# Kernel tuning notes

Measured on AMD Instinct MI355X. Metric: run time of the kernel, lower is better.

## Reference

```python
import jax, jax.numpy as jnp
import numpy as np

B, TOPK, MN = 128, 32, 64
MAX_NODES, H, E = 256, 128, 128
N_ENT, N_REL = 40000, 400


def setup_inputs() -> dict:
    key = jax.random.key(0)
    ks = jax.random.split(key, 11)
    s = 0.02  # weight init scale
    return {
        "node_embeddings": jax.random.normal(ks[0], (B, MAX_NODES + 2, H), jnp.float32),
        "entity_table": jax.random.normal(ks[1], (N_ENT, E), jnp.float32) * s,
        "relation_table": jax.random.normal(ks[2], (N_REL, E), jnp.float32) * s,
        "W_ih": jax.random.normal(ks[3], (3 * H, 2 * E), jnp.float32) * s,
        "W_hh": jax.random.normal(ks[4], (3 * H, H), jnp.float32) * s,
        "b_ih": jax.random.normal(ks[5], (3 * H,), jnp.float32) * s,
        "b_hh": jax.random.normal(ks[6], (3 * H,), jnp.float32) * s,
        "aim_nodes": jax.random.randint(ks[7], (B, TOPK), 0, MAX_NODES),
        "aim_entities": jax.random.randint(ks[8], (B, TOPK), 0, N_ENT),
        "neighbors": jax.random.randint(ks[9], (B, TOPK, MN, 2), 0, MAX_NODES + 2),
        "neighbors_num": jax.random.randint(ks[10], (B, TOPK), 0, MN + 1),
    }


def reference(node_embeddings, entity_table, relation_table, W_ih, W_hh, b_ih, b_hh,
              aim_nodes, aim_entities, neighbors, neighbors_num):
    # Agent.aggregate with use_rnn=True; returns updated node_embeddings.
    b, topk, mn, _ = neighbors.shape
    h_dim = node_embeddings.shape[-1]
    nb_nodes = neighbors[..., 0]      # (B, topk, mn) node positions
    nb_rel = neighbors[..., 1]        # (B, topk, mn) relation ids

    # per-batch gather of hidden states of neighbor nodes -> (B, topk, mn, H)
    h = jnp.take_along_axis(node_embeddings,
                            nb_nodes.reshape(b, topk * mn)[:, :, None],
                            axis=1).reshape(b, topk, mn, h_dim)
    ent = entity_table[aim_entities]          # (B, topk, E)
    rel = relation_table[nb_rel]              # (B, topk, mn, E)
    # GRU input: concat(aim entity embedding broadcast over neighbors, relation emb)
    x = jnp.concatenate(
        [jnp.broadcast_to(ent[:, :, None, :], rel.shape), rel], axis=-1)  # (B,topk,mn,2E)

    # torch GRUCell: gates ordered (r, z, n)
    gi = jnp.einsum('btme,ge->btmg', x, W_ih) + b_ih  # (B,topk,mn,3H)
    gh = jnp.einsum('btmh,gh->btmg', h, W_hh) + b_hh
    i_r, i_z, i_n = jnp.split(gi, 3, axis=-1)
    h_r, h_z, h_n = jnp.split(gh, 3, axis=-1)
    r = jax.nn.sigmoid(i_r + h_r)
    z = jax.nn.sigmoid(i_z + h_z)
    n = jnp.tanh(i_n + r * h_n)
    h_new = (1.0 - z) * n + z * h              # (B,topk,mn,H)

    # masked mean over valid neighbors (masked_fill(0) then sum / max(num,1))
    mask = jnp.arange(mn)[None, None, :] < neighbors_num[:, :, None]
    denom = neighbors_num.astype(h_new.dtype) + (neighbors_num == 0).astype(h_new.dtype)
    upd = jnp.where(mask[..., None], h_new, 0.0).sum(axis=2) / denom[..., None]  # (B,topk,H)

    # scatter updated representations back into the node table
    bidx = jnp.arange(b)[:, None]
    return node_embeddings.at[bidx, aim_nodes].set(upd)
```

## Files before the change

kernel.cpp:

```cpp
#include <hip/hip_runtime.h>

#define BB     128
#define TOPK   32
#define MN     64
#define NODES  258
#define HD     128
#define G3     384
#define NREL   400
#define SEG1_OFF 448
#define SEG2_OFF 4544
#define NROWS_TOT 37568

typedef __bf16 bf16x8 __attribute__((ext_vector_type(8)));
typedef float  f32x4  __attribute__((ext_vector_type(4)));

__device__ inline unsigned short f2bf(float f) {
    unsigned u = __float_as_uint(f);
    u = (u + 0x7fff + ((u >> 16) & 1)) >> 16;
    return (unsigned short)u;
}
__device__ inline float bf2f(unsigned short s) {
    return __uint_as_float(((unsigned)s) << 16);
}
__device__ inline float fsig(float x) {
    float e = __builtin_amdgcn_exp2f(-1.442695041f * x);
    return __builtin_amdgcn_rcpf(1.f + e);
}
__device__ inline float ftanh(float x) {
    x = fminf(15.f, fmaxf(-15.f, x));
    float e = __builtin_amdgcn_exp2f(2.885390082f * x);
    return (e - 1.f) * __builtin_amdgcn_rcpf(e + 1.f);
}

__global__ __launch_bounds__(256) void pack_all(
        const float* __restrict__ node_emb, const float* __restrict__ ent_tab,
        const float* __restrict__ rel_tab, const int* __restrict__ aim_ent,
        unsigned short* __restrict__ A, float* __restrict__ out) {
    int i = blockIdx.x * 256 + threadIdx.x;
    int row = i >> 7, k = i & 127;
    float v;
    if (row < NREL)            v = rel_tab[i];
    else if (row < SEG1_OFF)   v = 0.f;
    else if (row < SEG2_OFF)   v = ent_tab[(size_t)aim_ent[row - SEG1_OFF] * 128 + k];
    else {
        int n = row - SEG2_OFF;
        v = node_emb[(size_t)n * 128 + k];
        out[(size_t)n * 128 + k] = v;
    }
    A[i] = f2bf(v);
}

__global__ __launch_bounds__(256) void pack_w(
        const float* __restrict__ W_ih, const float* __restrict__ W_hh,
        const float* __restrict__ b_ih, const float* __restrict__ b_hh,
        unsigned short* __restrict__ Wpack, float* __restrict__ biasb) {
    int i = blockIdx.x * 256 + threadIdx.x;
    int s = i / 49152, r = i % 49152;
    int n = r >> 7, k = r & 127;
    float v;
    if (s == 0)      v = W_ih[n * 256 + 128 + k];
    else if (s == 1) v = W_ih[n * 256 + k];
    else             v = W_hh[n * 128 + k];
    Wpack[i] = f2bf(v);
    if (i < 3 * 384) {
        int s2 = i / 384, g = i % 384;
        biasb[i] = (s2 == 0) ? 0.f : (s2 == 1 ? b_ih[g] : b_hh[g]);
    }
}

__global__ __launch_bounds__(256) void mfma_gemm(
        const unsigned short* __restrict__ A, const unsigned short* __restrict__ Wpack,
        const float* __restrict__ biasb, unsigned short* __restrict__ G) {
    const int w = threadIdx.x >> 6, lane = threadIdx.x & 63;
    const int row0 = blockIdx.x * 64 + w * 16;
    const int seg  = (row0 < SEG1_OFF) ? 0 : (row0 < SEG2_OFF ? 1 : 2);
    const unsigned short* Wt = Wpack + (size_t)seg * 384 * 128;
    const int limit = (seg == 0) ? NREL : NROWS_TOT;

    const int koff  = (lane >> 4) << 3;
    const int arow  = row0 + (lane & 15);
    const int rbase = row0 + ((lane >> 4) << 2);
    bf16x8 a[4];
#pragma unroll
    for (int kb = 0; kb < 4; ++kb)
        a[kb] = *reinterpret_cast<const bf16x8*>(A + (size_t)arow * 128 + kb * 32 + koff);

#pragma unroll 2
    for (int t = 0; t < 24; ++t) {
        const int bcol = t * 16 + (lane & 15);
        bf16x8 bf[4];
#pragma unroll
        for (int kb = 0; kb < 4; ++kb)
            bf[kb] = *reinterpret_cast<const bf16x8*>(Wt + (size_t)bcol * 128 + kb * 32 + koff);
        f32x4 acc = {0.f, 0.f, 0.f, 0.f};
#pragma unroll
        for (int kb = 0; kb < 4; ++kb)
            acc = __builtin_amdgcn_mfma_f32_16x16x32_bf16(a[kb], bf[kb], acc, 0, 0, 0);
        const float bv = biasb[seg * 384 + bcol];
#pragma unroll
        for (int i = 0; i < 4; ++i) {
            int grow = rbase + i;
            if (grow < limit) G[(size_t)grow * 384 + bcol] = f2bf(acc[i] + bv);
        }
    }
}

__global__ __launch_bounds__(128) void gru_agg(
        const float* __restrict__ node_emb, const unsigned short* __restrict__ G,
        const int* __restrict__ aim_nodes, const int* __restrict__ neighbors,
        const int* __restrict__ nb_num, float* __restrict__ out) {
    const int bt = blockIdx.x;
    const int b = bt >> 5, t = bt & 31;
    const int h = threadIdx.x;

    const int myaim = aim_nodes[bt];
    for (int t2 = t + 1; t2 < TOPK; ++t2)
        if (aim_nodes[b * TOPK + t2] == myaim) return;

    __shared__ int2 nbs[MN];
    if (h < MN) nbs[h] = ((const int2*)(neighbors + (size_t)bt * MN * 2))[h];
    __syncthreads();

    const size_t erow = (size_t)(SEG1_OFF + bt) * 384;
    const float ge_r = bf2f(G[erow + h]);
    const float ge_z = bf2f(G[erow + 128 + h]);
    const float ge_n = bf2f(G[erow + 256 + h]);

    int num = nb_num[bt];
    num = (num < 0) ? 0 : (num > MN ? MN : num);

    const unsigned short* ghb = G + (size_t)(SEG2_OFF + b * NODES) * 384;
    const float* heb = node_emb + (size_t)b * NODES * 128;

    float acc = 0.f;
    int m = 0;
    for (; m + 4 <= num; m += 4) {
        float gr_r[4], gr_z[4], gr_n[4], h_r[4], h_z[4], h_n[4], hv[4];
#pragma unroll
        for (int j = 0; j < 4; ++j) {
            int2 p = nbs[m + j];
            const unsigned short* gr = G + (size_t)p.y * 384;
            const unsigned short* gh = ghb + (size_t)p.x * 384;
            gr_r[j] = bf2f(gr[h]); gr_z[j] = bf2f(gr[128 + h]); gr_n[j] = bf2f(gr[256 + h]);
            h_r[j]  = bf2f(gh[h]); h_z[j]  = bf2f(gh[128 + h]); h_n[j]  = bf2f(gh[256 + h]);
            hv[j]   = heb[(size_t)p.x * 128 + h];
        }
#pragma unroll
        for (int j = 0; j < 4; ++j) {
            float r = fsig(ge_r + gr_r[j] + h_r[j]);
            float z = fsig(ge_z + gr_z[j] + h_z[j]);
            float n = ftanh(ge_n + gr_n[j] + r * h_n[j]);
            acc += (1.f - z) * n + z * hv[j];
        }
    }
    for (; m < num; ++m) {
        int2 p = nbs[m];
        const unsigned short* gr = G + (size_t)p.y * 384;
        const unsigned short* gh = ghb + (size_t)p.x * 384;
        float r = fsig(ge_r + bf2f(gr[h]) + bf2f(gh[h]));
        float z = fsig(ge_z + bf2f(gr[128 + h]) + bf2f(gh[128 + h]));
        float n = ftanh(ge_n + bf2f(gr[256 + h]) + r * bf2f(gh[256 + h]));
        acc += (1.f - z) * n + z * heb[(size_t)p.x * 128 + h];
    }
    const float denom = (num > 0) ? (float)num : 1.f;
    out[((size_t)b * NODES + myaim) * 128 + h] = acc * __builtin_amdgcn_rcpf(denom);
}

extern "C" void kernel_launch(void* const* d_in, const int* in_sizes, int n_in,
                              void* d_out, int out_size, void* d_ws, size_t ws_size,
                              hipStream_t stream) {
    const float* node_emb = (const float*)d_in[0];
    const float* ent_tab  = (const float*)d_in[1];
    const float* rel_tab  = (const float*)d_in[2];
    const float* W_ih     = (const float*)d_in[3];
    const float* W_hh     = (const float*)d_in[4];
    const float* b_ih     = (const float*)d_in[5];
    const float* b_hh     = (const float*)d_in[6];
    const int* aim_nodes  = (const int*)d_in[7];
    const int* aim_ent    = (const int*)d_in[8];
    const int* neighbors  = (const int*)d_in[9];
    const int* nb_num     = (const int*)d_in[10];
    float* out = (float*)d_out;

    unsigned short* G     = (unsigned short*)d_ws;
    unsigned short* A     = G + (size_t)NROWS_TOT * 384;
    unsigned short* Wpack = A + (size_t)NROWS_TOT * 128;
    float*          biasb = (float*)(Wpack + 3 * 384 * 128);

    hipLaunchKernelGGL(pack_all, dim3(NROWS_TOT * 128 / 256), dim3(256), 0, stream,
                       node_emb, ent_tab, rel_tab, aim_ent, A, out);
    hipLaunchKernelGGL(pack_w, dim3(3 * 384 * 128 / 256), dim3(256), 0, stream,
                       W_ih, W_hh, b_ih, b_hh, Wpack, biasb);
    hipLaunchKernelGGL(mfma_gemm, dim3(NROWS_TOT / 64), dim3(256), 0, stream,
                       A, Wpack, biasb, G);
    hipLaunchKernelGGL(gru_agg, dim3(BB * TOPK), dim3(128), 0, stream,
                       node_emb, G, aim_nodes, neighbors, nb_num, out);
}
```

Measured before the change: 180.5 us.

## Stage weight tiles in LDS and vectorize the packing kernel

The GEMM now processes 128-row tiles with each wave computing 32 rows, and splits the 384 output columns across 3 blocks. Each block stages its 128x128 bf16 weight slice in shared memory in an MFMA-friendly order, so weights are read from LDS instead of being refetched from global memory per wave. The pack kernel now uses float4 loads and 16-byte stores of eight bf16 values. The A buffer is padded to a multiple of 128 rows, which moves the workspace offset of Wpack. Each block uses 32KB of LDS, which limits occupancy.

```diff
diff --git a/kernel.cpp b/kernel.cpp
--- a/kernel.cpp
+++ b/kernel.cpp
@@ -10,6 +10,8 @@
 #define SEG1_OFF 448
 #define SEG2_OFF 4544
 #define NROWS_TOT 37568
+#define ROWPAD   37632
+#define COLSPLIT 3
 
 typedef __bf16 bf16x8 __attribute__((ext_vector_type(8)));
 typedef float  f32x4  __attribute__((ext_vector_type(4)));
@@ -37,17 +39,26 @@
         const float* __restrict__ rel_tab, const int* __restrict__ aim_ent,
         unsigned short* __restrict__ A, float* __restrict__ out) {
     int i = blockIdx.x * 256 + threadIdx.x;
-    int row = i >> 7, k = i & 127;
-    float v;
-    if (row < NREL)            v = rel_tab[i];
-    else if (row < SEG1_OFF)   v = 0.f;
-    else if (row < SEG2_OFF)   v = ent_tab[(size_t)aim_ent[row - SEG1_OFF] * 128 + k];
-    else {
+    int row = i >> 4, kc = (i & 15) << 3;
+    float4 v0 = {0.f,0.f,0.f,0.f}, v1 = {0.f,0.f,0.f,0.f};
+    if (row < NREL) {
+        const float4* p = (const float4*)(rel_tab + (size_t)row * 128 + kc);
+        v0 = p[0]; v1 = p[1];
+    } else if (row < SEG1_OFF) {
+    } else if (row < SEG2_OFF) {
+        const float* e = ent_tab + (size_t)aim_ent[row - SEG1_OFF] * 128 + kc;
+        v0 = ((const float4*)e)[0]; v1 = ((const float4*)e)[1];
+    } else if (row < NROWS_TOT) {
         int n = row - SEG2_OFF;
-        v = node_emb[(size_t)n * 128 + k];
-        out[(size_t)n * 128 + k] = v;
-    }
-    A[i] = f2bf(v);
+        const float4* p = (const float4*)(node_emb + (size_t)n * 128 + kc);
+        v0 = p[0]; v1 = p[1];
+        float4* o = (float4*)(out + (size_t)n * 128 + kc);
+        o[0] = v0; o[1] = v1;
+    }
+    union { unsigned short s[8]; uint4 v; } u;
+    u.s[0]=f2bf(v0.x); u.s[1]=f2bf(v0.y); u.s[2]=f2bf(v0.z); u.s[3]=f2bf(v0.w);
+    u.s[4]=f2bf(v1.x); u.s[5]=f2bf(v1.y); u.s[6]=f2bf(v1.z); u.s[7]=f2bf(v1.w);
+    *(uint4*)(A + (size_t)row * 128 + kc) = u.v;
 }
 
 __global__ __launch_bounds__(256) void pack_w(
@@ -71,36 +82,63 @@
 __global__ __launch_bounds__(256) void mfma_gemm(
         const unsigned short* __restrict__ A, const unsigned short* __restrict__ Wpack,
         const float* __restrict__ biasb, unsigned short* __restrict__ G) {
-    const int w = threadIdx.x >> 6, lane = threadIdx.x & 63;
-    const int row0 = blockIdx.x * 64 + w * 16;
+    __shared__ __align__(16) unsigned short Bs[128 * 128];
+    const int tid = threadIdx.x;
+    const int w = tid >> 6, lane = tid & 63;
+    const int rb = blockIdx.x / COLSPLIT, cs = blockIdx.x % COLSPLIT;
+    const int row0 = rb * 128 + w * 32;
     const int seg  = (row0 < SEG1_OFF) ? 0 : (row0 < SEG2_OFF ? 1 : 2);
-    const unsigned short* Wt = Wpack + (size_t)seg * 384 * 128;
     const int limit = (seg == 0) ? NREL : NROWS_TOT;
-
-    const int koff  = (lane >> 4) << 3;
-    const int arow  = row0 + (lane & 15);
-    const int rbase = row0 + ((lane >> 4) << 2);
-    bf16x8 a[4];
-#pragma unroll
-    for (int kb = 0; kb < 4; ++kb)
-        a[kb] = *reinterpret_cast<const bf16x8*>(A + (size_t)arow * 128 + kb * 32 + koff);
-
+    const int colbase = cs * 128;
+    const unsigned short* Wt = Wpack + (size_t)seg * 49152 + (size_t)colbase * 128;
+
+#pragma unroll
+    for (int ii = 0; ii < 8; ++ii) {
+        int dst = ii * 256 + tid;
+        int g = dst >> 6, rem = dst & 63;
+        int qq = rem >> 4, cc = rem & 15;
+        int tt = g >> 2, kbb = g & 3;
+        uint4 v = *(const uint4*)(Wt + (size_t)(tt * 16 + cc) * 128 + kbb * 32 + qq * 8);
+        *(uint4*)(Bs + dst * 8) = v;
+    }
+
+    const int q = lane >> 4, c = lane & 15;
+    const int koff = q << 3;
+    bf16x8 a0[4], a1[4];
+    {
+        const unsigned short* Ar0 = A + (size_t)(row0 + c) * 128 + koff;
+        const unsigned short* Ar1 = Ar0 + 16 * 128;
+#pragma unroll
+        for (int kb = 0; kb < 4; ++kb) {
+            a0[kb] = *(const bf16x8*)(Ar0 + kb * 32);
+            a1[kb] = *(const bf16x8*)(Ar1 + kb * 32);
+        }
+    }
+    float bv[8];
+#pragma unroll
+    for (int t = 0; t < 8; ++t)
+        bv[t] = biasb[seg * 384 + colbase + t * 16 + c];
+
+    __syncthreads();
+
+    const int r0 = row0 + q * 4, r1 = r0 + 16;
 #pragma unroll 2
-    for (int t = 0; t < 24; ++t) {
-        const int bcol = t * 16 + (lane & 15);
+    for (int t = 0; t < 8; ++t) {
         bf16x8 bf[4];
 #pragma unroll
         for (int kb = 0; kb < 4; ++kb)
-            bf[kb] = *reinterpret_cast<const bf16x8*>(Wt + (size_t)bcol * 128 + kb * 32 + koff);
-        f32x4 acc = {0.f, 0.f, 0.f, 0.f};
-#pragma unroll
-        for (int kb = 0; kb < 4; ++kb)
-            acc = __builtin_amdgcn_mfma_f32_16x16x32_bf16(a[kb], bf[kb], acc, 0, 0, 0);
-        const float bv = biasb[seg * 384 + bcol];
-#pragma unroll
-        for (int i = 0; i < 4; ++i) {
-            int grow = rbase + i;
-            if (grow < limit) G[(size_t)grow * 384 + bcol] = f2bf(acc[i] + bv);
+            bf[kb] = *(const bf16x8*)(Bs + (size_t)((t * 4 + kb) * 64 + lane) * 8);
+        f32x4 acc0 = {0.f,0.f,0.f,0.f}, acc1 = {0.f,0.f,0.f,0.f};
+#pragma unroll
+        for (int kb = 0; kb < 4; ++kb) {
+            acc0 = __builtin_amdgcn_mfma_f32_16x16x32_bf16(a0[kb], bf[kb], acc0, 0, 0, 0);
+            acc1 = __builtin_amdgcn_mfma_f32_16x16x32_bf16(a1[kb], bf[kb], acc1, 0, 0, 0);
+        }
+        const int gc = colbase + t * 16 + c;
+#pragma unroll
+        for (int i2 = 0; i2 < 4; ++i2) {
+            if (r0 + i2 < limit) G[(size_t)(r0 + i2) * 384 + gc] = f2bf(acc0[i2] + bv[t]);
+            if (r1 + i2 < limit) G[(size_t)(r1 + i2) * 384 + gc] = f2bf(acc1[i2] + bv[t]);
         }
     }
 }
@@ -184,14 +222,14 @@
 
     unsigned short* G     = (unsigned short*)d_ws;
     unsigned short* A     = G + (size_t)NROWS_TOT * 384;
-    unsigned short* Wpack = A + (size_t)NROWS_TOT * 128;
+    unsigned short* Wpack = A + (size_t)ROWPAD * 128;
     float*          biasb = (float*)(Wpack + 3 * 384 * 128);
 
-    hipLaunchKernelGGL(pack_all, dim3(NROWS_TOT * 128 / 256), dim3(256), 0, stream,
+    hipLaunchKernelGGL(pack_all, dim3(ROWPAD * 16 / 256), dim3(256), 0, stream,
                        node_emb, ent_tab, rel_tab, aim_ent, A, out);
     hipLaunchKernelGGL(pack_w, dim3(3 * 384 * 128 / 256), dim3(256), 0, stream,
                        W_ih, W_hh, b_ih, b_hh, Wpack, biasb);
-    hipLaunchKernelGGL(mfma_gemm, dim3(NROWS_TOT / 64), dim3(256), 0, stream,
+    hipLaunchKernelGGL(mfma_gemm, dim3((ROWPAD / 128) * COLSPLIT), dim3(256), 0, stream,
                        A, Wpack, biasb, G);
     hipLaunchKernelGGL(gru_agg, dim3(BB * TOPK), dim3(128), 0, stream,
                        node_emb, G, aim_nodes, neighbors, nb_num, out);
```

New measurement: 151.3 us. 1.19x faster.
